# Performance work log

Hardware: AMD Instinct MI355X
Metric: run time of the kernel (lower is better)

The kernel has to match this reference:

```python
import jax, jax.numpy as jnp
import numpy as np

GRID_SIZE = 10
DEGREE = 3


def bspline_basis(x, grid_size=GRID_SIZE, degree=DEGREE):
    """Cox-de Boor B-spline basis on a uniform grid over [-1, 1].
    x: (...,) -> (..., grid_size + degree)
    """
    h = 2.0 / grid_size
    # extended knot vector, length grid_size + 2*degree + 1
    knots = jnp.arange(-degree, grid_size + degree + 1, dtype=x.dtype) * h - 1.0
    # keep inputs inside the grid support (standard KAN practice)
    x = jnp.clip(x, -1.0, 1.0 - 1e-6)
    xe = x[..., None]
    b = ((xe >= knots[:-1]) & (xe < knots[1:])).astype(x.dtype)  # degree-0, (..., K-1)
    for d in range(1, degree + 1):
        left = (xe - knots[: -(d + 1)]) / (knots[d:-1] - knots[: -(d + 1)]) * b[..., :-1]
        right = (knots[d + 1:] - xe) / (knots[d + 1:] - knots[1:-d]) * b[..., 1:]
        b = left + right
    return b  # (..., grid_size + degree)


def setup_inputs() -> dict:
    key = jax.random.key(0)
    k1, k2, k3 = jax.random.split(key, 3)
    B, S, IN, OUT, E = 4, 2048, 256, 256, 8
    n_basis = GRID_SIZE + DEGREE
    x = jax.random.normal(k1, (B, S, IN), dtype=jnp.float32)
    coeff = jax.random.normal(k2, (E, n_basis), dtype=jnp.float32) * 0.1
    gating_weights = jax.random.normal(k3, (IN, OUT, E), dtype=jnp.float32)
    return {"x": x, "coeff": coeff, "gating_weights": gating_weights}


def reference(x, coeff, gating_weights):
    # spline experts: elementwise basis eval, then per-expert linear combo
    basis = bspline_basis(x)                              # (B, S, I, n_basis)
    expert_outputs = jnp.einsum('bsin,en->bsie', basis, coeff)  # (B, S, I, E)
    gates = jax.nn.softmax(gating_weights, axis=-1)       # (I, O, E)
    out = jnp.einsum('bsie,ioe->bso', expert_outputs, gates)
    return out
```

## Files before the change

### kernel.cpp

```cpp
#include <hip/hip_runtime.h>

typedef __attribute__((ext_vector_type(8))) short short8;
typedef __attribute__((ext_vector_type(4))) float f32x4;

#define IN_DIM 256
#define OUT_DIM 256
#define NB 16
#define KDIM (IN_DIM * NB)
#define TM 128
#define TN 128
#define BK 64
#define LDA 72
#define KSPLIT 4
#define IPER (IN_DIM / KSPLIT)
#define STEPS (IPER / 4)

__device__ __forceinline__ unsigned short f2bf(float f) {
  union { float f; unsigned int u; } v; v.f = f;
  unsigned int r = v.u + 0x7fffu + ((v.u >> 16) & 1u);
  return (unsigned short)(r >> 16);
}

__device__ __forceinline__ void spline_row(float xv, unsigned short* rowp) {
  float xc = fminf(fmaxf(xv, -1.0f), 1.0f - 1e-6f);
  float u = (xc + 1.0f) * 5.0f;
  int c = (int)u;
  c = c > 9 ? 9 : (c < 0 ? 0 : c);
  float tt = u - (float)c;
  float omt = 1.0f - tt;
  float t2 = tt * tt, t3 = t2 * tt;
  float b0 = omt * omt * omt * (1.0f / 6.0f);
  float b1 = (3.0f * t3 - 6.0f * t2 + 4.0f) * (1.0f / 6.0f);
  float b2 = (-3.0f * t3 + 3.0f * t2 + 3.0f * tt + 1.0f) * (1.0f / 6.0f);
  float b3 = t3 * (1.0f / 6.0f);
  unsigned h0 = f2bf(b0), h1 = f2bf(b1), h2 = f2bf(b2), h3 = f2bf(b3);
  const int a = c >> 1;
  const bool odd = (c & 1) != 0;
  unsigned p01 = h0 | (h1 << 16);
  unsigned p23 = h2 | (h3 << 16);
  unsigned A0 = odd ? (h0 << 16) : p01;
  unsigned A1 = odd ? (h1 | (h2 << 16)) : p23;
  unsigned A2 = odd ? h3 : 0u;
  unsigned d[8];
#pragma unroll
  for (int j = 0; j < 8; ++j) {
    unsigned v = (j == a) ? A0 : 0u;
    v = (j == a + 1) ? A1 : v;
    v = (j == a + 2) ? A2 : v;
    d[j] = v;
  }
  *(int4*)&rowp[0] = *(const int4*)&d[0];
  *(int4*)&rowp[8] = *(const int4*)&d[4];
}

__global__ __launch_bounds__(256) void kan_prep(const float* __restrict__ coeff,
                                                const float* __restrict__ gw,
                                                unsigned short* __restrict__ BmT,
                                                float* __restrict__ out) {
  __shared__ float csh[104];
  __shared__ unsigned short tile[16][256];
  const int t = threadIdx.x;
  {
    const int bid = blockIdx.y * 16 + blockIdx.x;
    float4 z; z.x = z.y = z.z = z.w = 0.f;
    float4* ob = (float4*)out;
#pragma unroll
    for (int j = 0; j < 8; ++j) ob[(size_t)bid * 2048 + j * 256 + t] = z;
  }
  if (t < 104) csh[t] = coeff[t];
  __syncthreads();
  const int otile = blockIdx.x, itile = blockIdx.y;
  const int il = t >> 4, ol = t & 15;
  const int i = itile * 16 + il;
  const int o = otile * 16 + ol;
  const float* g = gw + (size_t)(i * OUT_DIM + o) * 8;
  float4 g0 = *(const float4*)g;
  float4 g1 = *(const float4*)(g + 4);
  float ge[8] = {g0.x, g0.y, g0.z, g0.w, g1.x, g1.y, g1.z, g1.w};
  float mx = ge[0];
#pragma unroll
  for (int e = 1; e < 8; ++e) mx = fmaxf(mx, ge[e]);
  float p[8]; float s = 0.f;
#pragma unroll
  for (int e = 0; e < 8; ++e) { p[e] = __expf(ge[e] - mx); s += p[e]; }
  const float inv = 1.0f / s;
  unsigned short row[16];
#pragma unroll
  for (int n = 0; n < 13; ++n) {
    float w = 0.f;
#pragma unroll
    for (int e = 0; e < 8; ++e) w += p[e] * csh[e * 13 + n];
    row[n] = f2bf(w * inv);
  }
  row[13] = 0; row[14] = 0; row[15] = 0;
  int4* dst = (int4*)&tile[ol][il * 16];
  dst[0] = *(const int4*)&row[0];
  dst[1] = *(const int4*)&row[8];
  __syncthreads();
  const int oo = t >> 4, ck = t & 15;
  int4 v0 = *(const int4*)&tile[oo][ck * 16];
  int4 v1 = *(const int4*)&tile[oo][ck * 16 + 8];
  int4* out4 = (int4*)(BmT + (size_t)(otile * 16 + oo) * KDIM + itile * 256 + ck * 16);
  out4[0] = v0;
  out4[1] = v1;
}

__global__ __launch_bounds__(256, 2) void kan_gemm(const float* __restrict__ x,
                                                   const unsigned short* __restrict__ BmT,
                                                   float* __restrict__ out) {
  __shared__ unsigned short AshB[2][TM * LDA];
  __shared__ unsigned short BshB[2][TN * LDA];

  const int t = threadIdx.x;
  const int lane = t & 63;
  const int wave = t >> 6;
  const int wm = wave & 1, wn = wave >> 1;
  const int mb = blockIdx.x * TM;
  const int ob = blockIdx.y * TN;
  const int i0 = blockIdx.z * IPER;

  const int r = t & 127;
  const int ph = t >> 7;
  const float* xrow = x + (size_t)(mb + r) * IN_DIM + i0 + 2 * ph;
  const int adst = r * LDA + 2 * ph * NB;

  const unsigned short* bsrc[4];
  int bdst[4];
#pragma unroll
  for (int q = 0; q < 4; ++q) {
    int olo = (t >> 3) + 32 * q;
    bsrc[q] = BmT + (size_t)(ob + olo) * KDIM + i0 * NB + (t & 7) * 8;
    bdst[q] = olo * LDA + (t & 7) * 8;
  }

  f32x4 acc[4][4];
#pragma unroll
  for (int a = 0; a < 4; ++a)
#pragma unroll
    for (int b = 0; b < 4; ++b) acc[a][b] = (f32x4){0.f, 0.f, 0.f, 0.f};

  int aoff[4], boff[4];
#pragma unroll
  for (int f = 0; f < 4; ++f) {
    aoff[f] = (wm * 64 + f * 16 + (lane & 15)) * LDA + (lane >> 4) * 8;
    boff[f] = (wn * 64 + f * 16 + (lane & 15)) * LDA + (lane >> 4) * 8;
  }

  {
    float2 x0 = *(const float2*)xrow;
    int4 breg[4];
#pragma unroll
    for (int q = 0; q < 4; ++q) breg[q] = *(const int4*)(bsrc[q]);
#pragma unroll
    for (int q = 0; q < 4; ++q) *(int4*)&BshB[0][bdst[q]] = breg[q];
    spline_row(x0.x, &AshB[0][adst]);
    spline_row(x0.y, &AshB[0][adst + NB]);
  }

  for (int s = 0; s < STEPS; ++s) {
    __syncthreads();
    const int cur = s & 1;
    const bool more = (s + 1 < STEPS);
    int4 breg[4];
    float2 xn;
    if (more) {
#pragma unroll
      for (int q = 0; q < 4; ++q) breg[q] = *(const int4*)(bsrc[q] + (s + 1) * BK);
      xn = *(const float2*)(xrow + (s + 1) * 4);
    }
    const unsigned short* Ac = AshB[cur];
    const unsigned short* Bc = BshB[cur];
#pragma unroll
    for (int kc = 0; kc < 2; ++kc) {
      short8 af[4], bfr[4];
#pragma unroll
      for (int f = 0; f < 4; ++f) af[f] = *(const short8*)&Ac[aoff[f] + kc * 32];
#pragma unroll
      for (int f = 0; f < 4; ++f) bfr[f] = *(const short8*)&Bc[boff[f] + kc * 32];
#pragma unroll
      for (int mf = 0; mf < 4; ++mf)
#pragma unroll
        for (int nf = 0; nf < 4; ++nf)
          acc[mf][nf] = __builtin_amdgcn_mfma_f32_16x16x32_bf16(af[mf], bfr[nf], acc[mf][nf], 0, 0, 0);
    }
    if (more) {
      unsigned short* An = AshB[1 - cur];
      unsigned short* Bn = BshB[1 - cur];
#pragma unroll
      for (int q = 0; q < 4; ++q) *(int4*)&Bn[bdst[q]] = breg[q];
      spline_row(xn.x, An + adst);
      spline_row(xn.y, An + adst + NB);
    }
  }

#pragma unroll
  for (int mf = 0; mf < 4; ++mf)
#pragma unroll
    for (int nf = 0; nf < 4; ++nf)
#pragma unroll
      for (int q = 0; q < 4; ++q) {
        int row = mb + wm * 64 + mf * 16 + ((lane >> 4) << 2) + q;
        int col = ob + wn * 64 + nf * 16 + (lane & 15);
        atomicAdd(out + (size_t)row * OUT_DIM + col, acc[mf][nf][q]);
      }
}

extern "C" void kernel_launch(void* const* d_in, const int* in_sizes, int n_in,
                              void* d_out, int out_size, void* d_ws, size_t ws_size,
                              hipStream_t stream) {
  const float* x     = (const float*)d_in[0];
  const float* coeff = (const float*)d_in[1];
  const float* gw    = (const float*)d_in[2];
  float* out = (float*)d_out;
  unsigned short* BmT = (unsigned short*)d_ws;

  kan_prep<<<dim3(16, 16), dim3(256), 0, stream>>>(coeff, gw, BmT, out);
  dim3 grid(8192 / TM, OUT_DIM / TN, KSPLIT);
  kan_gemm<<<grid, dim3(256), 0, stream>>>(x, BmT, out);
}
```

Baseline: 112.6 us.

## Use direct global-to-LDS loads with XOR-swizzled shared layout in GEMM

Replaces register-staged B and x loads with global_load_lds direct-to-LDS transfers, and changes the padded shared layout to an XOR-swizzled unpadded layout to avoid bank conflicts. x values are staged in LDS in advance and spline rows are built from them. s_setprio is raised around the MFMA block. The aim is to cut VGPR pressure and load latency. In exchange, synchronisation now relies on barriers covering asynchronous LDS writes, which adds correctness risk.

```diff
diff --git a/kernel.cpp b/kernel.cpp
--- a/kernel.cpp
+++ b/kernel.cpp
@@ -10,7 +10,6 @@
 #define TM 128
 #define TN 128
 #define BK 64
-#define LDA 72
 #define KSPLIT 4
 #define IPER (IN_DIM / KSPLIT)
 #define STEPS (IPER / 4)
@@ -21,7 +20,12 @@
   return (unsigned short)(r >> 16);
 }
 
-__device__ __forceinline__ void spline_row(float xv, unsigned short* rowp) {
+__device__ __forceinline__ void glds16(const void* g, void* l) {
+  __builtin_amdgcn_global_load_lds((__attribute__((address_space(1))) const void*)g,
+                                   (__attribute__((address_space(3))) void*)l, 16, 0, 0);
+}
+
+__device__ __forceinline__ void spline_row(float xv, unsigned* d) {
   float xc = fminf(fmaxf(xv, -1.0f), 1.0f - 1e-6f);
   float u = (xc + 1.0f) * 5.0f;
   int c = (int)u;
@@ -41,7 +45,6 @@
   unsigned A0 = odd ? (h0 << 16) : p01;
   unsigned A1 = odd ? (h1 | (h2 << 16)) : p23;
   unsigned A2 = odd ? h3 : 0u;
-  unsigned d[8];
 #pragma unroll
   for (int j = 0; j < 8; ++j) {
     unsigned v = (j == a) ? A0 : 0u;
@@ -49,8 +52,6 @@
     v = (j == a + 2) ? A2 : v;
     d[j] = v;
   }
-  *(int4*)&rowp[0] = *(const int4*)&d[0];
-  *(int4*)&rowp[8] = *(const int4*)&d[4];
 }
 
 __global__ __launch_bounds__(256) void kan_prep(const float* __restrict__ coeff,
@@ -105,11 +106,27 @@
   out4[1] = v1;
 }
 
+#define STAGE_A(snext, buf) do {                                                   \
+    const int p_ = (snext) & 1, h_ = ((snext) >> 1) & 1;                           \
+    const char* xb_ = (const char*)&Xsh[0][0] + h_ * 4096;                         \
+    float2 xv_ = *(const float2*)(xb_ + r * 32 + ((p_ ^ (r & 1)) << 4) + ph * 8);  \
+    char* ab_ = (char*)&Ash[0][0] + (buf) * 16384 + r * 128;                       \
+    const int m_ = r & 7;                                                          \
+    unsigned d_[8];                                                                \
+    spline_row(xv_.x, d_);                                                         \
+    *(int4*)(ab_ + (((4 * ph + 0) ^ m_) << 4)) = *(const int4*)&d_[0];             \
+    *(int4*)(ab_ + (((4 * ph + 1) ^ m_) << 4)) = *(const int4*)&d_[4];             \
+    spline_row(xv_.y, d_);                                                         \
+    *(int4*)(ab_ + (((4 * ph + 2) ^ m_) << 4)) = *(const int4*)&d_[0];             \
+    *(int4*)(ab_ + (((4 * ph + 3) ^ m_) << 4)) = *(const int4*)&d_[4];             \
+  } while (0)
+
 __global__ __launch_bounds__(256, 2) void kan_gemm(const float* __restrict__ x,
                                                    const unsigned short* __restrict__ BmT,
                                                    float* __restrict__ out) {
-  __shared__ unsigned short AshB[2][TM * LDA];
-  __shared__ unsigned short BshB[2][TN * LDA];
+  __shared__ unsigned short Ash[2][TM * BK];
+  __shared__ unsigned short Bsh[2][TN * BK];
+  __shared__ float Xsh[2][TM * 8];
 
   const int t = threadIdx.x;
   const int lane = t & 63;
@@ -121,17 +138,14 @@
 
   const int r = t & 127;
   const int ph = t >> 7;
-  const float* xrow = x + (size_t)(mb + r) * IN_DIM + i0 + 2 * ph;
-  const int adst = r * LDA + 2 * ph * NB;
-
-  const unsigned short* bsrc[4];
-  int bdst[4];
-#pragma unroll
-  for (int q = 0; q < 4; ++q) {
-    int olo = (t >> 3) + 32 * q;
-    bsrc[q] = BmT + (size_t)(ob + olo) * KDIM + i0 * NB + (t & 7) * 8;
-    bdst[q] = olo * LDA + (t & 7) * 8;
-  }
+
+  const int jsw = (t & 7) ^ ((t >> 3) & 7);
+  const unsigned short* bgbase = BmT + (size_t)(ob + (t >> 3)) * KDIM + i0 * NB + jsw * 8;
+  const int csw = (t & 1) ^ ((t >> 1) & 1);
+  const float* xgbase = x + (size_t)(mb + (t >> 1)) * IN_DIM + i0 + csw * 4;
+
+  char* const bl = (char*)&Bsh[0][0] + wave * 1024;
+  char* const xl = (char*)&Xsh[0][0] + wave * 1024;
 
   f32x4 acc[4][4];
 #pragma unroll
@@ -142,55 +156,51 @@
   int aoff[4], boff[4];
 #pragma unroll
   for (int f = 0; f < 4; ++f) {
-    aoff[f] = (wm * 64 + f * 16 + (lane & 15)) * LDA + (lane >> 4) * 8;
-    boff[f] = (wn * 64 + f * 16 + (lane & 15)) * LDA + (lane >> 4) * 8;
-  }
-
-  {
-    float2 x0 = *(const float2*)xrow;
-    int4 breg[4];
-#pragma unroll
-    for (int q = 0; q < 4; ++q) breg[q] = *(const int4*)(bsrc[q]);
-#pragma unroll
-    for (int q = 0; q < 4; ++q) *(int4*)&BshB[0][bdst[q]] = breg[q];
-    spline_row(x0.x, &AshB[0][adst]);
-    spline_row(x0.y, &AshB[0][adst + NB]);
-  }
+    const int ro = wm * 64 + f * 16 + (lane & 15);
+    aoff[f] = ro * 128 + ((((lane >> 4)) ^ (ro & 7)) << 4);
+    const int bo = wn * 64 + f * 16 + (lane & 15);
+    boff[f] = bo * 128 + ((((lane >> 4)) ^ (bo & 7)) << 4);
+  }
+
+  glds16(xgbase, xl);
+#pragma unroll
+  for (int q = 0; q < 4; ++q)
+    glds16(bgbase + (size_t)q * 32 * KDIM, bl + q * 4096);
+  asm volatile("s_waitcnt vmcnt(0)" ::: "memory");
+  __syncthreads();
+  STAGE_A(0, 0);
 
   for (int s = 0; s < STEPS; ++s) {
     __syncthreads();
     const int cur = s & 1;
-    const bool more = (s + 1 < STEPS);
-    int4 breg[4];
-    float2 xn;
-    if (more) {
-#pragma unroll
-      for (int q = 0; q < 4; ++q) breg[q] = *(const int4*)(bsrc[q] + (s + 1) * BK);
-      xn = *(const float2*)(xrow + (s + 1) * 4);
+    if (s + 1 < STEPS) {
+#pragma unroll
+      for (int q = 0; q < 4; ++q)
+        glds16(bgbase + (size_t)(s + 1) * BK + (size_t)q * 32 * KDIM,
+               bl + (1 - cur) * 16384 + q * 4096);
     }
-    const unsigned short* Ac = AshB[cur];
-    const unsigned short* Bc = BshB[cur];
+    if (((s & 1) == 0) && (s + 2 < STEPS)) {
+      const int g = (s >> 1) + 1;
+      glds16(xgbase + g * 8, xl + (g & 1) * 4096);
+    }
+    const char* Ac = (const char*)&Ash[0][0] + cur * 16384;
+    const char* Bc = (const char*)&Bsh[0][0] + cur * 16384;
+    __builtin_amdgcn_s_setprio(1);
 #pragma unroll
     for (int kc = 0; kc < 2; ++kc) {
       short8 af[4], bfr[4];
 #pragma unroll
-      for (int f = 0; f < 4; ++f) af[f] = *(const short8*)&Ac[aoff[f] + kc * 32];
-#pragma unroll
-      for (int f = 0; f < 4; ++f) bfr[f] = *(const short8*)&Bc[boff[f] + kc * 32];
+      for (int f = 0; f < 4; ++f) af[f] = *(const short8*)(Ac + (aoff[f] ^ (kc << 6)));
+#pragma unroll
+      for (int f = 0; f < 4; ++f) bfr[f] = *(const short8*)(Bc + (boff[f] ^ (kc << 6)));
 #pragma unroll
       for (int mf = 0; mf < 4; ++mf)
 #pragma unroll
         for (int nf = 0; nf < 4; ++nf)
           acc[mf][nf] = __builtin_amdgcn_mfma_f32_16x16x32_bf16(af[mf], bfr[nf], acc[mf][nf], 0, 0, 0);
     }
-    if (more) {
-      unsigned short* An = AshB[1 - cur];
-      unsigned short* Bn = BshB[1 - cur];
-#pragma unroll
-      for (int q = 0; q < 4; ++q) *(int4*)&Bn[bdst[q]] = breg[q];
-      spline_row(xn.x, An + adst);
-      spline_row(xn.y, An + adst + NB);
-    }
+    __builtin_amdgcn_s_setprio(0);
+    if (s + 1 < STEPS) STAGE_A(s + 1, 1 - cur);
   }
 
 #pragma unroll
```

After: 114.1 us. No clear change (+1.4%).
